# Optimization experiments

Measured on AMD Instinct MI355X. Metric: run time of the kernel, lower is better.

Reference implementation:

```python
import jax, jax.numpy as jnp
import numpy as np

B, L, H, D = 8, 4800, 8, 64  # L = 60*80 tokens, D = head_dim = self.dim


def setup_inputs() -> dict:
    key = jax.random.key(0)
    ks = jax.random.split(key, 8)
    q = jax.random.normal(ks[0], (B, L, H, D), jnp.float32)
    k = jax.random.normal(ks[1], (B, L, H, D), jnp.float32)
    v = jax.random.normal(ks[2], (B, L, H, D), jnp.float32)
    temperature = jnp.ones((H, 1, 1), jnp.float32)          # nn.Parameter(torch.ones(H,1,1))
    attns = jnp.ones((4,), jnp.float32)                      # four scalar gate params (init 1.0)
    # Conv1d(dim,1,k=1): weight [1, dim, 1] -> store as [dim]; bias [1]
    row_w = 0.1 * jax.random.normal(ks[3], (D,), jnp.float32)
    row_b = 0.1 * jax.random.normal(ks[4], (1,), jnp.float32)
    col_w = 0.1 * jax.random.normal(ks[5], (D,), jnp.float32)
    col_b = 0.1 * jax.random.normal(ks[6], (1,), jnp.float32)
    return {"q": q, "k": k, "v": v, "temperature": temperature, "attns": attns,
            "row_w": row_w, "row_b": row_b, "col_w": col_w, "col_b": col_b}


def _l2norm(x):
    # torch F.normalize(dim=-1): x / max(||x||, eps)
    n = jnp.sqrt(jnp.sum(x * x, axis=-1, keepdims=True))
    return x / jnp.maximum(n, 1e-12)


def reference(q, k, v, temperature, attns, row_w, row_b, col_w, col_b):
    # [B,L,H,D] -> [B,H,D,L]
    qt = _l2norm(q.transpose(0, 2, 3, 1))
    kt = _l2norm(k.transpose(0, 2, 3, 1))
    vt = v.transpose(0, 2, 3, 1)
    # channel attention: [B,H,D,D]
    attn = jnp.einsum('bhdl,bhel->bhde', qt, kt)
    # col_conv: Conv1d over C1 rows -> gate per column; row_conv: over C2 -> gate per row
    w_col = jax.nn.sigmoid(jnp.einsum('bhce,c->bhe', attn, col_w) + col_b)[:, :, None, :]  # [B,H,1,C]
    w_row = jax.nn.sigmoid(jnp.einsum('bhce,e->bhc', attn, row_w) + row_b)[:, :, :, None]  # [B,H,C,1]
    attn = (attn * w_col + attn * w_row) * temperature[None]  # temperature [H,1,1] broadcasts
    C = attn.shape[-1]
    neg_inf = jnp.array(-jnp.inf, attn.dtype)
    out = jnp.zeros_like(vt)  # [B,H,D,L]
    for i, tk in enumerate([C // 2, (2 * C) // 3, (3 * C) // 4, (4 * C) // 5]):
        thr = jax.lax.top_k(attn, tk)[0][..., -1:]           # kth largest per row
        a = jnp.where(attn >= thr, attn, neg_inf)            # keep top-k entries
        a = jax.nn.softmax(a, axis=-1)
        out = out + attns[i] * jnp.einsum('bhde,bhel->bhdl', a, vt)
    # rearrange 'b head c (h w) -> b (head c) h w' then back to [B, L, head, c]
    return out.transpose(0, 3, 1, 2)  # [B,L,H,D]
```

## Files before the change

### kernel.cpp

```cpp
#include <hip/hip_runtime.h>

#define B_ 8
#define L_ 4800
#define H_ 8
#define D_ 64
#define BH_ 64

#define NCH 15
#define CHUNK 320
#define SLAB 8
#define WSLABS 10

#define GP_SIZE   (BH_*NCH*4096)
#define QSQP_OFF  GP_SIZE
#define QSQP_SIZE (BH_*NCH*64)
#define KSQP_OFF  (QSQP_OFF + QSQP_SIZE)
#define M_OFF     (KSQP_OFF + QSQP_SIZE)

__global__ __launch_bounds__(256) void gram_kernel(
    const float* __restrict__ q, const float* __restrict__ k,
    float* __restrict__ Gp, float* __restrict__ qsqp, float* __restrict__ ksqp)
{
  const int bh = blockIdx.y;
  const int b = bh >> 3, h = bh & 7;
  const int cx = blockIdx.x;
  const int l0 = cx * CHUNK;
  const int t = threadIdx.x;
  const int w = t >> 6, lane = t & 63;

  __shared__ float Ls[4][2][2][SLAB][64];

  const int lrow = lane >> 4;
  const int lcol = (lane & 15) * 4;
  const int r0 = (lane >> 3) * 8;
  const int c0 = (lane & 7) * 8;

  const float* qb = q + (size_t)(b*L_)*512 + h*64;
  const float* kb = k + (size_t)(b*L_)*512 + h*64;

  float accG[8][8] = {};
  float sqq[4] = {0,0,0,0}, sqk[4] = {0,0,0,0};

  {
    const int ls = l0 + w*SLAB;
    const float* qp = qb + (size_t)(ls + lrow)*512 + lcol;
    const float* kp = kb + (size_t)(ls + lrow)*512 + lcol;
    float4 a0 = *(const float4*)qp;
    float4 a1 = *(const float4*)(qp + 4*512);
    float4 b0 = *(const float4*)kp;
    float4 b1 = *(const float4*)(kp + 4*512);
    sqq[0]+=a0.x*a0.x; sqq[1]+=a0.y*a0.y; sqq[2]+=a0.z*a0.z; sqq[3]+=a0.w*a0.w;
    sqq[0]+=a1.x*a1.x; sqq[1]+=a1.y*a1.y; sqq[2]+=a1.z*a1.z; sqq[3]+=a1.w*a1.w;
    sqk[0]+=b0.x*b0.x; sqk[1]+=b0.y*b0.y; sqk[2]+=b0.z*b0.z; sqk[3]+=b0.w*b0.w;
    sqk[0]+=b1.x*b1.x; sqk[1]+=b1.y*b1.y; sqk[2]+=b1.z*b1.z; sqk[3]+=b1.w*b1.w;
    *(float4*)&Ls[w][0][0][lrow  ][lcol] = a0;
    *(float4*)&Ls[w][0][0][lrow+4][lcol] = a1;
    *(float4*)&Ls[w][0][1][lrow  ][lcol] = b0;
    *(float4*)&Ls[w][0][1][lrow+4][lcol] = b1;
  }

  for (int s = 0; s < WSLABS; s++) {
    const int cur = s & 1;
    float4 a0, a1, b0, b1;
    if (s + 1 < WSLABS) {
      const int ls = l0 + (w + 4*(s+1))*SLAB;
      const float* qp = qb + (size_t)(ls + lrow)*512 + lcol;
      const float* kp = kb + (size_t)(ls + lrow)*512 + lcol;
      a0 = *(const float4*)qp;
      a1 = *(const float4*)(qp + 4*512);
      b0 = *(const float4*)kp;
      b1 = *(const float4*)(kp + 4*512);
    }
    const float (*Lq)[64] = Ls[w][cur][0];
    const float (*Lk)[64] = Ls[w][cur][1];
#pragma unroll
    for (int r = 0; r < SLAB; r++) {
      float4 qa0 = *(const float4*)&Lq[r][r0];
      float4 qa1 = *(const float4*)&Lq[r][r0+4];
      float4 kb0 = *(const float4*)&Lk[r][c0];
      float4 kb1 = *(const float4*)&Lk[r][c0+4];
      float av[8] = {qa0.x,qa0.y,qa0.z,qa0.w,qa1.x,qa1.y,qa1.z,qa1.w};
      float bv[8] = {kb0.x,kb0.y,kb0.z,kb0.w,kb1.x,kb1.y,kb1.z,kb1.w};
#pragma unroll
      for (int i = 0; i < 8; i++)
#pragma unroll
        for (int j = 0; j < 8; j++)
          accG[i][j] = fmaf(av[i], bv[j], accG[i][j]);
    }
    if (s + 1 < WSLABS) {
      sqq[0]+=a0.x*a0.x; sqq[1]+=a0.y*a0.y; sqq[2]+=a0.z*a0.z; sqq[3]+=a0.w*a0.w;
      sqq[0]+=a1.x*a1.x; sqq[1]+=a1.y*a1.y; sqq[2]+=a1.z*a1.z; sqq[3]+=a1.w*a1.w;
      sqk[0]+=b0.x*b0.x; sqk[1]+=b0.y*b0.y; sqk[2]+=b0.z*b0.z; sqk[3]+=b0.w*b0.w;
      sqk[0]+=b1.x*b1.x; sqk[1]+=b1.y*b1.y; sqk[2]+=b1.z*b1.z; sqk[3]+=b1.w*b1.w;
      *(float4*)&Ls[w][cur^1][0][lrow  ][lcol] = a0;
      *(float4*)&Ls[w][cur^1][0][lrow+4][lcol] = a1;
      *(float4*)&Ls[w][cur^1][1][lrow  ][lcol] = b0;
      *(float4*)&Ls[w][cur^1][1][lrow+4][lcol] = b1;
    }
  }

  float* red = &Ls[0][0][0][0][0];
  float4* redf4 = (float4*)red;
  float* gout = Gp + ((size_t)bh*NCH + cx)*4096;

  __syncthreads();
  if (r0 < 32) {
#pragma unroll
    for (int i = 0; i < 8; i++) {
      *(float4*)&red[w*2048 + (r0+i)*64 + c0    ] = make_float4(accG[i][0],accG[i][1],accG[i][2],accG[i][3]);
      *(float4*)&red[w*2048 + (r0+i)*64 + c0 + 4] = make_float4(accG[i][4],accG[i][5],accG[i][6],accG[i][7]);
    }
  }
  __syncthreads();
#pragma unroll
  for (int pp = 0; pp < 2; pp++) {
    int fi = t + pp*256;
    float4 s0 = redf4[fi], s1 = redf4[512+fi], s2 = redf4[1024+fi], s3 = redf4[1536+fi];
    float4 r; r.x = s0.x+s1.x+s2.x+s3.x; r.y = s0.y+s1.y+s2.y+s3.y;
    r.z = s0.z+s1.z+s2.z+s3.z; r.w = s0.w+s1.w+s2.w+s3.w;
    *(float4*)&gout[fi*4] = r;
  }
  __syncthreads();
  if (r0 >= 32) {
#pragma unroll
    for (int i = 0; i < 8; i++) {
      *(float4*)&red[w*2048 + (r0-32+i)*64 + c0    ] = make_float4(accG[i][0],accG[i][1],accG[i][2],accG[i][3]);
      *(float4*)&red[w*2048 + (r0-32+i)*64 + c0 + 4] = make_float4(accG[i][4],accG[i][5],accG[i][6],accG[i][7]);
    }
  }
  __syncthreads();
#pragma unroll
  for (int pp = 0; pp < 2; pp++) {
    int fi = t + pp*256;
    float4 s0 = redf4[fi], s1 = redf4[512+fi], s2 = redf4[1024+fi], s3 = redf4[1536+fi];
    float4 r; r.x = s0.x+s1.x+s2.x+s3.x; r.y = s0.y+s1.y+s2.y+s3.y;
    r.z = s0.z+s1.z+s2.z+s3.z; r.w = s0.w+s1.w+s2.w+s3.w;
    *(float4*)&gout[2048 + fi*4] = r;
  }
  __syncthreads();
  redf4[w*64 + lane]       = make_float4(sqq[0],sqq[1],sqq[2],sqq[3]);
  redf4[256 + w*64 + lane] = make_float4(sqk[0],sqk[1],sqk[2],sqk[3]);
  __syncthreads();
  if (t < 128) {
    const int d = t & 63;
    const int col4 = d >> 2, c = d & 3;
    const int base = (t < 64) ? 0 : 1024;
    float s = 0.f;
#pragma unroll
    for (int ww = 0; ww < 4; ww++)
#pragma unroll
      for (int m = 0; m < 4; m++)
        s += red[base + (ww*64 + m*16 + col4)*4 + c];
    float* dst = (t < 64) ? qsqp : ksqp;
    dst[((size_t)bh*NCH + cx)*64 + d] = s;
  }
}

__global__ __launch_bounds__(256) void mask_kernel(
    const float* __restrict__ Gp, const float* __restrict__ qsqp,
    const float* __restrict__ ksqp,
    const float* __restrict__ temperature, const float* __restrict__ attns,
    const float* __restrict__ row_w, const float* __restrict__ row_b,
    const float* __restrict__ col_w, const float* __restrict__ col_b,
    float* __restrict__ M)
{
  const int bh = blockIdx.x;
  const int h = bh & 7;
  const int t = threadIdx.x;
  const int d = t & 63, q4 = t >> 6;
  const int e0 = q4 * 16;

  __shared__ float att[64][65];
  __shared__ float rnq[64], rnk[64], cw[64], rw[64];
  __shared__ float wcol[64], wrow[64];
  __shared__ float thr[4][64];
  __shared__ float pmax[4][64];
  __shared__ float rowmax[64];
  __shared__ float psum[4][4][64];
  __shared__ float rinv[4][64];

  if (t < 64) {
    float s = 0.f;
    for (int c = 0; c < NCH; c++) s += qsqp[((size_t)bh*NCH + c)*64 + t];
    rnq[t] = 1.0f / fmaxf(sqrtf(s), 1e-12f);
  } else if (t < 128) {
    float s = 0.f;
    for (int c = 0; c < NCH; c++) s += ksqp[((size_t)bh*NCH + c)*64 + (t-64)];
    rnk[t-64] = 1.0f / fmaxf(sqrtf(s), 1e-12f);
  } else if (t < 192) {
    cw[t-128] = col_w[t-128];
  } else {
    rw[t-192] = row_w[t-192];
  }
  __syncthreads();

  {
    const float rq = rnq[d];
#pragma unroll
    for (int ee = 0; ee < 16; ee += 4) {
      float4 g = make_float4(0.f,0.f,0.f,0.f);
      for (int c = 0; c < NCH; c++) {
        float4 gc = *(const float4*)&Gp[((size_t)bh*NCH + c)*4096 + d*64 + e0 + ee];
        g.x += gc.x; g.y += gc.y; g.z += gc.z; g.w += gc.w;
      }
      att[d][e0+ee+0] = g.x * rq * rnk[e0+ee+0];
      att[d][e0+ee+1] = g.y * rq * rnk[e0+ee+1];
      att[d][e0+ee+2] = g.z * rq * rnk[e0+ee+2];
      att[d][e0+ee+3] = g.w * rq * rnk[e0+ee+3];
    }
  }
  __syncthreads();

  if (t < 64) {
    float s = 0.f;
    for (int c = 0; c < 64; c++) s += att[c][t] * cw[c];
    s += col_b[0];
    wcol[t] = 1.0f / (1.0f + __expf(-s));
  } else if (t < 128) {
    int c = t - 64;
    float s = 0.f;
    for (int e = 0; e < 64; e++) s += att[c][e] * rw[e];
    s += row_b[0];
    wrow[c] = 1.0f / (1.0f + __expf(-s));
  }
  __syncthreads();

  {
    const float temp = temperature[h];
    const float wr = wrow[d];
    float mx = -1e30f;
#pragma unroll
    for (int ee = 0; ee < 16; ee++) {
      float x = att[d][e0+ee] * ((wcol[e0+ee] + wr) * temp);
      att[d][e0+ee] = x;
      mx = fmaxf(mx, x);
    }
    pmax[q4][d] = mx;
  }
  __syncthreads();
  if (t < 64)
    rowmax[t] = fmaxf(fmaxf(pmax[0][t], pmax[1][t]), fmaxf(pmax[2][t], pmax[3][t]));

  {
    float x[16];
#pragma unroll
    for (int j = 0; j < 16; j++) x[j] = att[d][e0+j];
    int gt[16] = {}, ge[16] = {};
    for (int m = 0; m < 64; m++) {
      float y = att[d][m];
#pragma unroll
      for (int j = 0; j < 16; j++) { gt[j] += (y > x[j]); ge[j] += (y >= x[j]); }
    }
    const int tks[4] = {32, 42, 48, 51};
#pragma unroll
    for (int j = 0; j < 16; j++)
#pragma unroll
      for (int i = 0; i < 4; i++)
        if (gt[j] <= tks[i]-1 && ge[j] >= tks[i]) thr[i][d] = x[j];
  }
  __syncthreads();

  {
    const float rm = rowmax[d];
    const float t0 = thr[0][d], t1 = thr[1][d], t2 = thr[2][d], t3 = thr[3][d];
    float s0=0.f, s1=0.f, s2=0.f, s3=0.f;
#pragma unroll
    for (int ee = 0; ee < 16; ee++) {
      float xv = att[d][e0+ee];
      float ex = __expf(xv - rm);
      if (xv >= t0) s0 += ex;
      if (xv >= t1) s1 += ex;
      if (xv >= t2) s2 += ex;
      if (xv >= t3) s3 += ex;
    }
    psum[q4][0][d] = s0; psum[q4][1][d] = s1; psum[q4][2][d] = s2; psum[q4][3][d] = s3;
  }
  __syncthreads();
  if (t < 64) {
#pragma unroll
    for (int i = 0; i < 4; i++) {
      float s = psum[0][i][t] + psum[1][i][t] + psum[2][i][t] + psum[3][i][t];
      rinv[i][t] = attns[i] / s;
    }
  }
  __syncthreads();

  {
    const float rm = rowmax[d];
    const float t0 = thr[0][d], t1 = thr[1][d], t2 = thr[2][d], t3 = thr[3][d];
    const float r0 = rinv[0][d], r1 = rinv[1][d], r2 = rinv[2][d], r3 = rinv[3][d];
    float* mo = M + (size_t)bh*4096 + d*64 + e0;
#pragma unroll
    for (int ee = 0; ee < 16; ee++) {
      float xv = att[d][e0+ee];
      float ex = __expf(xv - rm);
      float m = 0.f;
      if (xv >= t0) m += r0 * ex;
      if (xv >= t1) m += r1 * ex;
      if (xv >= t2) m += r2 * ex;
      if (xv >= t3) m += r3 * ex;
      mo[ee] = m;
    }
  }
}

__global__ __launch_bounds__(256) void apply_kernel(
    const float* __restrict__ M, const float* __restrict__ v,
    float* __restrict__ out)
{
  const int bh = blockIdx.y;
  const int b = bh >> 3, h = bh & 7;
  const int l0 = blockIdx.x * 64;
  const int t = threadIdx.x;

  __shared__ float Ms[64][68];
  __shared__ float Vs[64][68];

#pragma unroll
  for (int i = 0; i < 4; i++) {
    int idx = t + i*256;
    int dd = idx >> 4;
    int c4 = (idx & 15) * 4;
    float4 mv = *(const float4*)(M + (size_t)bh*4096 + dd*64 + c4);
    Ms[c4+0][dd] = mv.x; Ms[c4+1][dd] = mv.y; Ms[c4+2][dd] = mv.z; Ms[c4+3][dd] = mv.w;
    float4 vv = *(const float4*)(v + (((size_t)b*L_ + l0 + dd)*H_ + h)*D_ + c4);
    *(float4*)&Vs[dd][c4] = vv;
  }
  __syncthreads();

  const int dq = t & 15, lq = t >> 4;
  const int d0 = dq * 4, lr = lq * 4;
  float acc[4][4] = {};

#pragma unroll
  for (int e4 = 0; e4 < 16; e4++) {
    const int e = e4 * 4;
    float4 m0 = *(const float4*)&Ms[e+0][d0];
    float4 m1 = *(const float4*)&Ms[e+1][d0];
    float4 m2 = *(const float4*)&Ms[e+2][d0];
    float4 m3 = *(const float4*)&Ms[e+3][d0];
    float ma[4][4] = {{m0.x,m0.y,m0.z,m0.w},{m1.x,m1.y,m1.z,m1.w},
                      {m2.x,m2.y,m2.z,m2.w},{m3.x,m3.y,m3.z,m3.w}};
#pragma unroll
    for (int j = 0; j < 4; j++) {
      float4 vj = *(const float4*)&Vs[lr+j][e];
      float va[4] = {vj.x, vj.y, vj.z, vj.w};
#pragma unroll
      for (int i = 0; i < 4; i++) {
        acc[i][j] = fmaf(ma[0][i], va[0], acc[i][j]);
        acc[i][j] = fmaf(ma[1][i], va[1], acc[i][j]);
        acc[i][j] = fmaf(ma[2][i], va[2], acc[i][j]);
        acc[i][j] = fmaf(ma[3][i], va[3], acc[i][j]);
      }
    }
  }

#pragma unroll
  for (int j = 0; j < 4; j++) {
    int l = l0 + lr + j;
    float4 o = make_float4(acc[0][j], acc[1][j], acc[2][j], acc[3][j]);
    *(float4*)(out + (((size_t)b*L_ + l)*H_ + h)*D_ + d0) = o;
  }
}

extern "C" void kernel_launch(void* const* d_in, const int* in_sizes, int n_in,
                              void* d_out, int out_size, void* d_ws, size_t ws_size,
                              hipStream_t stream) {
  const float* q           = (const float*)d_in[0];
  const float* k           = (const float*)d_in[1];
  const float* v           = (const float*)d_in[2];
  const float* temperature = (const float*)d_in[3];
  const float* attns       = (const float*)d_in[4];
  const float* row_w       = (const float*)d_in[5];
  const float* row_b       = (const float*)d_in[6];
  const float* col_w       = (const float*)d_in[7];
  const float* col_b       = (const float*)d_in[8];
  float* out = (float*)d_out;

  float* ws   = (float*)d_ws;
  float* Gp   = ws;
  float* qsqp = ws + QSQP_OFF;
  float* ksqp = ws + KSQP_OFF;
  float* M    = ws + M_OFF;


  gram_kernel<<<dim3(NCH, BH_), 256, 0, stream>>>(q, k, Gp, qsqp, ksqp);
  mask_kernel<<<dim3(BH_), 256, 0, stream>>>(Gp, qsqp, ksqp, temperature, attns,
                                             row_w, row_b, col_w, col_b, M);
  apply_kernel<<<dim3(L_/64, BH_), 256, 0, stream>>>(M, v, out);
}
```

Baseline: 306.0 us.

## Restructure gram and apply kernels around full-row coalesced loads, add partial reduce

The gram kernel now uses 512-thread blocks per (position chunk, batch), loading contiguous 8-token rows across all 8 heads so global reads are fully coalesced. Each warp owns one head and writes its partial Gram matrix directly, with no intra-block reduction. A separate reduce kernel sums the per-chunk partials, so the mask kernel no longer loops over chunks. The apply kernel keeps a token's V row in registers and reads M through wave-uniform scalar loads, dropping shared-memory staging. The costs are a larger workspace, one extra launch, and heavy register use for the 64-float V row.

```diff
diff --git a/kernel.cpp b/kernel.cpp
--- a/kernel.cpp
+++ b/kernel.cpp
@@ -6,79 +6,66 @@
 #define D_ 64
 #define BH_ 64
 
-#define NCH 15
-#define CHUNK 320
-#define SLAB 8
-#define WSLABS 10
-
-#define GP_SIZE   (BH_*NCH*4096)
-#define QSQP_OFF  GP_SIZE
-#define QSQP_SIZE (BH_*NCH*64)
-#define KSQP_OFF  (QSQP_OFF + QSQP_SIZE)
-#define M_OFF     (KSQP_OFF + QSQP_SIZE)
-
-__global__ __launch_bounds__(256) void gram_kernel(
+__global__ __launch_bounds__(512, 4) void gram_kernel(
     const float* __restrict__ q, const float* __restrict__ k,
-    float* __restrict__ Gp, float* __restrict__ qsqp, float* __restrict__ ksqp)
+    float* __restrict__ Gp, float* __restrict__ qsqp, float* __restrict__ ksqp,
+    const int P, const int NS)
 {
-  const int bh = blockIdx.y;
-  const int b = bh >> 3, h = bh & 7;
-  const int cx = blockIdx.x;
-  const int l0 = cx * CHUNK;
+  const int p = blockIdx.x;
+  const int b = blockIdx.y;
   const int t = threadIdx.x;
-  const int w = t >> 6, lane = t & 63;
-
-  __shared__ float Ls[4][2][2][SLAB][64];
-
-  const int lrow = lane >> 4;
-  const int lcol = (lane & 15) * 4;
+  const int w = t >> 6;
+  const int lane = t & 63;
   const int r0 = (lane >> 3) * 8;
   const int c0 = (lane & 7) * 8;
-
-  const float* qb = q + (size_t)(b*L_)*512 + h*64;
-  const float* kb = k + (size_t)(b*L_)*512 + h*64;
+  const int to4 = t * 4;
+
+  __shared__ float Ls[2][2][8 * 512];
+
+  const size_t base = ((size_t)b * L_ + (size_t)p * NS * 8) * 512;
+  const float* qb = q + base;
+  const float* kb = k + base;
 
   float accG[8][8] = {};
-  float sqq[4] = {0,0,0,0}, sqk[4] = {0,0,0,0};
-
-  {
-    const int ls = l0 + w*SLAB;
-    const float* qp = qb + (size_t)(ls + lrow)*512 + lcol;
-    const float* kp = kb + (size_t)(ls + lrow)*512 + lcol;
-    float4 a0 = *(const float4*)qp;
-    float4 a1 = *(const float4*)(qp + 4*512);
-    float4 b0 = *(const float4*)kp;
-    float4 b1 = *(const float4*)(kp + 4*512);
-    sqq[0]+=a0.x*a0.x; sqq[1]+=a0.y*a0.y; sqq[2]+=a0.z*a0.z; sqq[3]+=a0.w*a0.w;
-    sqq[0]+=a1.x*a1.x; sqq[1]+=a1.y*a1.y; sqq[2]+=a1.z*a1.z; sqq[3]+=a1.w*a1.w;
-    sqk[0]+=b0.x*b0.x; sqk[1]+=b0.y*b0.y; sqk[2]+=b0.z*b0.z; sqk[3]+=b0.w*b0.w;
-    sqk[0]+=b1.x*b1.x; sqk[1]+=b1.y*b1.y; sqk[2]+=b1.z*b1.z; sqk[3]+=b1.w*b1.w;
-    *(float4*)&Ls[w][0][0][lrow  ][lcol] = a0;
-    *(float4*)&Ls[w][0][0][lrow+4][lcol] = a1;
-    *(float4*)&Ls[w][0][1][lrow  ][lcol] = b0;
-    *(float4*)&Ls[w][0][1][lrow+4][lcol] = b1;
-  }
-
-  for (int s = 0; s < WSLABS; s++) {
+  float sqq0=0.f,sqq1=0.f,sqq2=0.f,sqq3=0.f;
+  float sqk0=0.f,sqk1=0.f,sqk2=0.f,sqk3=0.f;
+
+  {
+    float4 a0 = *(const float4*)(qb + to4);
+    float4 a1 = *(const float4*)(qb + 2048 + to4);
+    float4 b0 = *(const float4*)(kb + to4);
+    float4 b1 = *(const float4*)(kb + 2048 + to4);
+    sqq0 += a0.x*a0.x; sqq1 += a0.y*a0.y; sqq2 += a0.z*a0.z; sqq3 += a0.w*a0.w;
+    sqq0 += a1.x*a1.x; sqq1 += a1.y*a1.y; sqq2 += a1.z*a1.z; sqq3 += a1.w*a1.w;
+    sqk0 += b0.x*b0.x; sqk1 += b0.y*b0.y; sqk2 += b0.z*b0.z; sqk3 += b0.w*b0.w;
+    sqk0 += b1.x*b1.x; sqk1 += b1.y*b1.y; sqk2 += b1.z*b1.z; sqk3 += b1.w*b1.w;
+    *(float4*)&Ls[0][0][to4] = a0;
+    *(float4*)&Ls[0][0][2048 + to4] = a1;
+    *(float4*)&Ls[0][1][to4] = b0;
+    *(float4*)&Ls[0][1][2048 + to4] = b1;
+  }
+  __syncthreads();
+
+  for (int s = 0; s < NS; s++) {
     const int cur = s & 1;
     float4 a0, a1, b0, b1;
-    if (s + 1 < WSLABS) {
-      const int ls = l0 + (w + 4*(s+1))*SLAB;
-      const float* qp = qb + (size_t)(ls + lrow)*512 + lcol;
-      const float* kp = kb + (size_t)(ls + lrow)*512 + lcol;
-      a0 = *(const float4*)qp;
-      a1 = *(const float4*)(qp + 4*512);
-      b0 = *(const float4*)kp;
-      b1 = *(const float4*)(kp + 4*512);
-    }
-    const float (*Lq)[64] = Ls[w][cur][0];
-    const float (*Lk)[64] = Ls[w][cur][1];
-#pragma unroll
-    for (int r = 0; r < SLAB; r++) {
-      float4 qa0 = *(const float4*)&Lq[r][r0];
-      float4 qa1 = *(const float4*)&Lq[r][r0+4];
-      float4 kb0 = *(const float4*)&Lk[r][c0];
-      float4 kb1 = *(const float4*)&Lk[r][c0+4];
+    const bool pf = (s + 1 < NS);
+    if (pf) {
+      const float* qp = qb + (size_t)(s + 1) * 4096;
+      const float* kp = kb + (size_t)(s + 1) * 4096;
+      a0 = *(const float4*)(qp + to4);
+      a1 = *(const float4*)(qp + 2048 + to4);
+      b0 = *(const float4*)(kp + to4);
+      b1 = *(const float4*)(kp + 2048 + to4);
+    }
+    const float* Lq = &Ls[cur][0][w * 64];
+    const float* Lk = &Ls[cur][1][w * 64];
+#pragma unroll
+    for (int r = 0; r < 8; r++) {
+      float4 qa0 = *(const float4*)(Lq + r * 512 + r0);
+      float4 qa1 = *(const float4*)(Lq + r * 512 + r0 + 4);
+      float4 kb0 = *(const float4*)(Lk + r * 512 + c0);
+      float4 kb1 = *(const float4*)(Lk + r * 512 + c0 + 4);
       float av[8] = {qa0.x,qa0.y,qa0.z,qa0.w,qa1.x,qa1.y,qa1.z,qa1.w};
       float bv[8] = {kb0.x,kb0.y,kb0.z,kb0.w,kb1.x,kb1.y,kb1.z,kb1.w};
 #pragma unroll
@@ -87,78 +74,108 @@
         for (int j = 0; j < 8; j++)
           accG[i][j] = fmaf(av[i], bv[j], accG[i][j]);
     }
-    if (s + 1 < WSLABS) {
-      sqq[0]+=a0.x*a0.x; sqq[1]+=a0.y*a0.y; sqq[2]+=a0.z*a0.z; sqq[3]+=a0.w*a0.w;
-      sqq[0]+=a1.x*a1.x; sqq[1]+=a1.y*a1.y; sqq[2]+=a1.z*a1.z; sqq[3]+=a1.w*a1.w;
-      sqk[0]+=b0.x*b0.x; sqk[1]+=b0.y*b0.y; sqk[2]+=b0.z*b0.z; sqk[3]+=b0.w*b0.w;
-      sqk[0]+=b1.x*b1.x; sqk[1]+=b1.y*b1.y; sqk[2]+=b1.z*b1.z; sqk[3]+=b1.w*b1.w;
-      *(float4*)&Ls[w][cur^1][0][lrow  ][lcol] = a0;
-      *(float4*)&Ls[w][cur^1][0][lrow+4][lcol] = a1;
-      *(float4*)&Ls[w][cur^1][1][lrow  ][lcol] = b0;
-      *(float4*)&Ls[w][cur^1][1][lrow+4][lcol] = b1;
-    }
-  }
-
-  float* red = &Ls[0][0][0][0][0];
-  float4* redf4 = (float4*)red;
-  float* gout = Gp + ((size_t)bh*NCH + cx)*4096;
-
-  __syncthreads();
-  if (r0 < 32) {
-#pragma unroll
-    for (int i = 0; i < 8; i++) {
-      *(float4*)&red[w*2048 + (r0+i)*64 + c0    ] = make_float4(accG[i][0],accG[i][1],accG[i][2],accG[i][3]);
-      *(float4*)&red[w*2048 + (r0+i)*64 + c0 + 4] = make_float4(accG[i][4],accG[i][5],accG[i][6],accG[i][7]);
-    }
-  }
-  __syncthreads();
-#pragma unroll
-  for (int pp = 0; pp < 2; pp++) {
-    int fi = t + pp*256;
-    float4 s0 = redf4[fi], s1 = redf4[512+fi], s2 = redf4[1024+fi], s3 = redf4[1536+fi];
-    float4 r; r.x = s0.x+s1.x+s2.x+s3.x; r.y = s0.y+s1.y+s2.y+s3.y;
-    r.z = s0.z+s1.z+s2.z+s3.z; r.w = s0.w+s1.w+s2.w+s3.w;
-    *(float4*)&gout[fi*4] = r;
-  }
-  __syncthreads();
-  if (r0 >= 32) {
-#pragma unroll
-    for (int i = 0; i < 8; i++) {
-      *(float4*)&red[w*2048 + (r0-32+i)*64 + c0    ] = make_float4(accG[i][0],accG[i][1],accG[i][2],accG[i][3]);
-      *(float4*)&red[w*2048 + (r0-32+i)*64 + c0 + 4] = make_float4(accG[i][4],accG[i][5],accG[i][6],accG[i][7]);
-    }
-  }
-  __syncthreads();
-#pragma unroll
-  for (int pp = 0; pp < 2; pp++) {
-    int fi = t + pp*256;
-    float4 s0 = redf4[fi], s1 = redf4[512+fi], s2 = redf4[1024+fi], s3 = redf4[1536+fi];
-    float4 r; r.x = s0.x+s1.x+s2.x+s3.x; r.y = s0.y+s1.y+s2.y+s3.y;
-    r.z = s0.z+s1.z+s2.z+s3.z; r.w = s0.w+s1.w+s2.w+s3.w;
-    *(float4*)&gout[2048 + fi*4] = r;
-  }
-  __syncthreads();
-  redf4[w*64 + lane]       = make_float4(sqq[0],sqq[1],sqq[2],sqq[3]);
-  redf4[256 + w*64 + lane] = make_float4(sqk[0],sqk[1],sqk[2],sqk[3]);
-  __syncthreads();
-  if (t < 128) {
-    const int d = t & 63;
-    const int col4 = d >> 2, c = d & 3;
-    const int base = (t < 64) ? 0 : 1024;
-    float s = 0.f;
-#pragma unroll
-    for (int ww = 0; ww < 4; ww++)
-#pragma unroll
-      for (int m = 0; m < 4; m++)
-        s += red[base + (ww*64 + m*16 + col4)*4 + c];
-    float* dst = (t < 64) ? qsqp : ksqp;
-    dst[((size_t)bh*NCH + cx)*64 + d] = s;
+    if (pf) {
+      sqq0 += a0.x*a0.x; sqq1 += a0.y*a0.y; sqq2 += a0.z*a0.z; sqq3 += a0.w*a0.w;
+      sqq0 += a1.x*a1.x; sqq1 += a1.y*a1.y; sqq2 += a1.z*a1.z; sqq3 += a1.w*a1.w;
+      sqk0 += b0.x*b0.x; sqk1 += b0.y*b0.y; sqk2 += b0.z*b0.z; sqk3 += b0.w*b0.w;
+      sqk0 += b1.x*b1.x; sqk1 += b1.y*b1.y; sqk2 += b1.z*b1.z; sqk3 += b1.w*b1.w;
+      *(float4*)&Ls[cur ^ 1][0][to4] = a0;
+      *(float4*)&Ls[cur ^ 1][0][2048 + to4] = a1;
+      *(float4*)&Ls[cur ^ 1][1][to4] = b0;
+      *(float4*)&Ls[cur ^ 1][1][2048 + to4] = b1;
+    }
+    __syncthreads();
+  }
+
+  float* gout = Gp + ((size_t)(b * 8 + w) * P + p) * 4096;
+#pragma unroll
+  for (int i = 0; i < 8; i++) {
+    *(float4*)(gout + (r0 + i) * 64 + c0) =
+        make_float4(accG[i][0], accG[i][1], accG[i][2], accG[i][3]);
+    *(float4*)(gout + (r0 + i) * 64 + c0 + 4) =
+        make_float4(accG[i][4], accG[i][5], accG[i][6], accG[i][7]);
+  }
+
+  float* S = &Ls[0][0][0];
+  *(float4*)(S + to4)        = make_float4(sqq0, sqq1, sqq2, sqq3);
+  *(float4*)(S + 2048 + to4) = make_float4(sqk0, sqk1, sqk2, sqk3);
+  __syncthreads();
+  if (t < 256) {
+    const int tensor = t >> 7;
+    const int C = t & 127;
+    const float* Sb = S + tensor * 2048;
+    float4 s0 = *(const float4*)(Sb + C * 4);
+    float4 s1 = *(const float4*)(Sb + (C + 128) * 4);
+    float4 s2 = *(const float4*)(Sb + (C + 256) * 4);
+    float4 s3 = *(const float4*)(Sb + (C + 384) * 4);
+    float4 r = make_float4(s0.x + s1.x + s2.x + s3.x,
+                           s0.y + s1.y + s2.y + s3.y,
+                           s0.z + s1.z + s2.z + s3.z,
+                           s0.w + s1.w + s2.w + s3.w);
+    const int h = C >> 4;
+    const int dd = (C & 15) * 4;
+    float* dst = tensor ? ksqp : qsqp;
+    *(float4*)(dst + ((size_t)(b * 8 + h) * P + p) * 64 + dd) = r;
+  }
+}
+
+__global__ __launch_bounds__(128) void reduce_kernel(
+    const float* __restrict__ Gp, const float* __restrict__ qsqp,
+    const float* __restrict__ ksqp, float* __restrict__ Gt,
+    float* __restrict__ qst, float* __restrict__ kst, const int P)
+{
+  const int j8 = blockIdx.x;
+  const int bh = blockIdx.y;
+  const int t = threadIdx.x;
+  const size_t off = (size_t)j8 * 512 + (size_t)t * 4;
+  const float* gp = Gp + (size_t)bh * P * 4096 + off;
+
+  float4 a0 = make_float4(0.f,0.f,0.f,0.f);
+  float4 a1 = make_float4(0.f,0.f,0.f,0.f);
+  float4 a2 = make_float4(0.f,0.f,0.f,0.f);
+  float4 a3 = make_float4(0.f,0.f,0.f,0.f);
+  int p = 0;
+  for (; p + 4 <= P; p += 4) {
+    float4 g0 = *(const float4*)(gp + (size_t)(p + 0) * 4096);
+    float4 g1 = *(const float4*)(gp + (size_t)(p + 1) * 4096);
+    float4 g2 = *(const float4*)(gp + (size_t)(p + 2) * 4096);
+    float4 g3 = *(const float4*)(gp + (size_t)(p + 3) * 4096);
+    a0.x += g0.x; a0.y += g0.y; a0.z += g0.z; a0.w += g0.w;
+    a1.x += g1.x; a1.y += g1.y; a1.z += g1.z; a1.w += g1.w;
+    a2.x += g2.x; a2.y += g2.y; a2.z += g2.z; a2.w += g2.w;
+    a3.x += g3.x; a3.y += g3.y; a3.z += g3.z; a3.w += g3.w;
+  }
+  for (; p < P; p++) {
+    float4 g = *(const float4*)(gp + (size_t)p * 4096);
+    a0.x += g.x; a0.y += g.y; a0.z += g.z; a0.w += g.w;
+  }
+  float4 r = make_float4(a0.x + a1.x + a2.x + a3.x,
+                         a0.y + a1.y + a2.y + a3.y,
+                         a0.z + a1.z + a2.z + a3.z,
+                         a0.w + a1.w + a2.w + a3.w);
+  *(float4*)(Gt + (size_t)bh * 4096 + off) = r;
+
+  if (j8 == 0) {
+    const int d2 = t & 63;
+    const float* sp = (t < 64) ? qsqp : ksqp;
+    const float* s = sp + (size_t)bh * P * 64 + d2;
+    float x0 = 0.f, x1 = 0.f, x2 = 0.f, x3 = 0.f;
+    int pp = 0;
+    for (; pp + 4 <= P; pp += 4) {
+      x0 += s[(size_t)(pp + 0) * 64];
+      x1 += s[(size_t)(pp + 1) * 64];
+      x2 += s[(size_t)(pp + 2) * 64];
+      x3 += s[(size_t)(pp + 3) * 64];
+    }
+    for (; pp < P; pp++) x0 += s[(size_t)pp * 64];
+    float* dst = (t < 64) ? qst : kst;
+    dst[bh * 64 + d2] = x0 + x1 + x2 + x3;
   }
 }
 
 __global__ __launch_bounds__(256) void mask_kernel(
-    const float* __restrict__ Gp, const float* __restrict__ qsqp,
-    const float* __restrict__ ksqp,
+    const float* __restrict__ Gt, const float* __restrict__ qst,
+    const float* __restrict__ kst,
     const float* __restrict__ temperature, const float* __restrict__ attns,
     const float* __restrict__ row_w, const float* __restrict__ row_b,
     const float* __restrict__ col_w, const float* __restrict__ col_b,
@@ -180,17 +197,13 @@
   __shared__ float rinv[4][64];
 
   if (t < 64) {
-    float s = 0.f;
-    for (int c = 0; c < NCH; c++) s += qsqp[((size_t)bh*NCH + c)*64 + t];
-    rnq[t] = 1.0f / fmaxf(sqrtf(s), 1e-12f);
+    rnq[t] = 1.0f / fmaxf(sqrtf(qst[bh * 64 + t]), 1e-12f);
   } else if (t < 128) {
-    float s = 0.f;
-    for (int c = 0; c < NCH; c++) s += ksqp[((size_t)bh*NCH + c)*64 + (t-64)];
-    rnk[t-64] = 1.0f / fmaxf(sqrtf(s), 1e-12f);
+    rnk[t - 64] = 1.0f / fmaxf(sqrtf(kst[bh * 64 + (t - 64)]), 1e-12f);
   } else if (t < 192) {
-    cw[t-128] = col_w[t-128];
+    cw[t - 128] = col_w[t - 128];
   } else {
-    rw[t-192] = row_w[t-192];
+    rw[t - 192] = row_w[t - 192];
   }
   __syncthreads();
 
@@ -198,11 +211,7 @@
     const float rq = rnq[d];
 #pragma unroll
     for (int ee = 0; ee < 16; ee += 4) {
-      float4 g = make_float4(0.f,0.f,0.f,0.f);
-      for (int c = 0; c < NCH; c++) {
-        float4 gc = *(const float4*)&Gp[((size_t)bh*NCH + c)*4096 + d*64 + e0 + ee];
-        g.x += gc.x; g.y += gc.y; g.z += gc.z; g.w += gc.w;
-      }
+      float4 g = *(const float4*)&Gt[(size_t)bh * 4096 + d * 64 + e0 + ee];
       att[d][e0+ee+0] = g.x * rq * rnk[e0+ee+0];
       att[d][e0+ee+1] = g.y * rq * rnk[e0+ee+1];
       att[d][e0+ee+2] = g.z * rq * rnk[e0+ee+2];
@@ -289,7 +298,7 @@
     const float rm = rowmax[d];
     const float t0 = thr[0][d], t1 = thr[1][d], t2 = thr[2][d], t3 = thr[3][d];
     const float r0 = rinv[0][d], r1 = rinv[1][d], r2 = rinv[2][d], r3 = rinv[3][d];
-    float* mo = M + (size_t)bh*4096 + d*64 + e0;
+    float* mo = M + (size_t)bh * 4096 + d * 64 + e0;
 #pragma unroll
     for (int ee = 0; ee < 16; ee++) {
       float xv = att[d][e0+ee];
@@ -304,62 +313,42 @@
   }
 }
 
-__global__ __launch_bounds__(256) void apply_kernel(
+__global__ __launch_bounds__(512, 4) void apply_kernel(
     const float* __restrict__ M, const float* __restrict__ v,
     float* __restrict__ out)
 {
-  const int bh = blockIdx.y;
-  const int b = bh >> 3, h = bh & 7;
-  const int l0 = blockIdx.x * 64;
+  const int lb = blockIdx.x;
+  const int b = blockIdx.y;
   const int t = threadIdx.x;
-
-  __shared__ float Ms[64][68];
-  __shared__ float Vs[64][68];
-
-#pragma unroll
-  for (int i = 0; i < 4; i++) {
-    int idx = t + i*256;
-    int dd = idx >> 4;
-    int c4 = (idx & 15) * 4;
-    float4 mv = *(const float4*)(M + (size_t)bh*4096 + dd*64 + c4);
-    Ms[c4+0][dd] = mv.x; Ms[c4+1][dd] = mv.y; Ms[c4+2][dd] = mv.z; Ms[c4+3][dd] = mv.w;
-    float4 vv = *(const float4*)(v + (((size_t)b*L_ + l0 + dd)*H_ + h)*D_ + c4);
-    *(float4*)&Vs[dd][c4] = vv;
-  }
-  __syncthreads();
-
-  const int dq = t & 15, lq = t >> 4;
-  const int d0 = dq * 4, lr = lq * 4;
-  float acc[4][4] = {};
-
-#pragma unroll
-  for (int e4 = 0; e4 < 16; e4++) {
-    const int e = e4 * 4;
-    float4 m0 = *(const float4*)&Ms[e+0][d0];
-    float4 m1 = *(const float4*)&Ms[e+1][d0];
-    float4 m2 = *(const float4*)&Ms[e+2][d0];
-    float4 m3 = *(const float4*)&Ms[e+3][d0];
-    float ma[4][4] = {{m0.x,m0.y,m0.z,m0.w},{m1.x,m1.y,m1.z,m1.w},
-                      {m2.x,m2.y,m2.z,m2.w},{m3.x,m3.y,m3.z,m3.w}};
-#pragma unroll
-    for (int j = 0; j < 4; j++) {
-      float4 vj = *(const float4*)&Vs[lr+j][e];
-      float va[4] = {vj.x, vj.y, vj.z, vj.w};
-#pragma unroll
-      for (int i = 0; i < 4; i++) {
-        acc[i][j] = fmaf(ma[0][i], va[0], acc[i][j]);
-        acc[i][j] = fmaf(ma[1][i], va[1], acc[i][j]);
-        acc[i][j] = fmaf(ma[2][i], va[2], acc[i][j]);
-        acc[i][j] = fmaf(ma[3][i], va[3], acc[i][j]);
+  const int w = __builtin_amdgcn_readfirstlane(t >> 6);
+  const int lane = t & 63;
+  const int l = lb * 64 + lane;
+
+  const float* vrow = v + ((size_t)(b * L_ + l) * 8 + w) * 64;
+  float vreg[64];
+#pragma unroll
+  for (int j = 0; j < 16; j++) {
+    float4 x = *(const float4*)(vrow + j * 4);
+    vreg[j*4+0] = x.x; vreg[j*4+1] = x.y; vreg[j*4+2] = x.z; vreg[j*4+3] = x.w;
+  }
+
+  const float* Mb = M + (size_t)(b * 8 + w) * 4096;
+  float* orow = out + ((size_t)(b * L_ + l) * 8 + w) * 64;
+
+  for (int dg = 0; dg < 16; dg++) {
+    const float* mr = Mb + dg * 256;
+    float ob[4];
+#pragma unroll
+    for (int r = 0; r < 4; r++) {
+      float a0 = 0.f, a1 = 0.f;
+#pragma unroll
+      for (int e = 0; e < 64; e += 2) {
+        a0 = fmaf(mr[r * 64 + e],     vreg[e],     a0);
+        a1 = fmaf(mr[r * 64 + e + 1], vreg[e + 1], a1);
       }
-    }
-  }
-
-#pragma unroll
-  for (int j = 0; j < 4; j++) {
-    int l = l0 + lr + j;
-    float4 o = make_float4(acc[0][j], acc[1][j], acc[2][j], acc[3][j]);
-    *(float4*)(out + (((size_t)b*L_ + l)*H_ + h)*D_ + d0) = o;
+      ob[r] = a0 + a1;
+    }
+    *(float4*)(orow + dg * 4) = make_float4(ob[0], ob[1], ob[2], ob[3]);
   }
 }
 
@@ -377,15 +366,28 @@
   const float* col_b       = (const float*)d_in[8];
   float* out = (float*)d_out;
 
-  float* ws   = (float*)d_ws;
+  auto needB = [](long long P) -> size_t {
+    return (size_t)(270336LL * P + 532480LL) * 4u;
+  };
+  int P = 60;
+  if (ws_size < needB(60)) P = 30;
+  if (ws_size < needB(30)) P = 15;
+  const int NS = 600 / P;
+
+  float* ws = (float*)d_ws;
+  const size_t GPs = (size_t)64 * P * 4096;
+  const size_t SQs = (size_t)64 * P * 64;
   float* Gp   = ws;
-  float* qsqp = ws + QSQP_OFF;
-  float* ksqp = ws + KSQP_OFF;
-  float* M    = ws + M_OFF;
-
-
-  gram_kernel<<<dim3(NCH, BH_), 256, 0, stream>>>(q, k, Gp, qsqp, ksqp);
-  mask_kernel<<<dim3(BH_), 256, 0, stream>>>(Gp, qsqp, ksqp, temperature, attns,
+  float* qsqp = Gp + GPs;
+  float* ksqp = qsqp + SQs;
+  float* Gt   = ksqp + SQs;
+  float* qst  = Gt + 262144;
+  float* kst  = qst + 4096;
+  float* M    = kst + 4096;
+
+  gram_kernel<<<dim3(P, B_), 512, 0, stream>>>(q, k, Gp, qsqp, ksqp, P, NS);
+  reduce_kernel<<<dim3(8, BH_), 128, 0, stream>>>(Gp, qsqp, ksqp, Gt, qst, kst, P);
+  mask_kernel<<<dim3(BH_), 256, 0, stream>>>(Gt, qst, kst, temperature, attns,
                                              row_w, row_b, col_w, col_b, M);
-  apply_kernel<<<dim3(L_/64, BH_), 256, 0, stream>>>(M, v, out);
-}
+  apply_kernel<<<dim3(L_ / 64, B_), 512, 0, stream>>>(M, v, out);
+}
```

Measured after the change: 1.037 ms. 239% more time.
